# Optimization experiments

Hardware: AMD Instinct MI355X
Metric: run time of the kernel (lower is better)

## Reference

```python
import jax, jax.numpy as jnp
import numpy as np

P_DROP = 0.7   # weights_dropout p
TAU = 0.95     # instance_dropout (gumbel-softmax temperature)


def _linear_init(key, fan_in, fan_out):
    k1, k2 = jax.random.split(key)
    bound = 1.0 / np.sqrt(fan_in)
    W = jax.random.uniform(k1, (fan_in, fan_out), minval=-bound, maxval=bound, dtype=jnp.float32)
    b = jax.random.uniform(k2, (fan_out,), minval=-bound, maxval=bound, dtype=jnp.float32)
    return W, b


def setup_inputs() -> dict:
    key = jax.random.key(0)
    ks = jax.random.split(key, 12)
    N, C, IND = 2048, 64, 512            # Nmol, Nconf, input feature dim
    HD1, HD2, HD3 = 256, 256, 128        # ndim[1:]
    DET1, DET2 = 128, 64                 # det_ndim
    W1, b1 = _linear_init(ks[0], IND, HD1)
    W2, b2 = _linear_init(ks[1], HD1, HD2)
    W3, b3 = _linear_init(ks[2], HD2, HD3)
    D1, db1 = _linear_init(ks[3], HD3, DET1)
    D2, db2 = _linear_init(ks[4], DET1, DET2)
    D3, db3 = _linear_init(ks[5], DET2, 1)
    E, eb = _linear_init(ks[6], HD3, 1)
    x = jax.random.normal(ks[7], (N, C, IND), dtype=jnp.float32)
    m = jnp.ones((N, C, 1), jnp.float32)
    u = jax.random.uniform(ks[8], (N, 1, C), minval=1e-6, maxval=1.0 - 1e-6, dtype=jnp.float32)
    return dict(x=x, m=m, u=u, W1=W1, b1=b1, W2=W2, b2=b2, W3=W3, b3=b3,
                D1=D1, db1=db1, D2=D2, db2=db2, D3=D3, db3=db3, E=E, eb=eb)


def _weights_dropout(w, p):
    # w: (N, 1, C). Zero the lowest p fraction per row, renormalize the rest
    # with a softmax over the kept values (faithful to WeightsDropout.forward).
    N, _, C = w.shape
    k = int(C * p)
    w2 = w[:, 0, :]                                   # (N, C)
    idx = jnp.argsort(w2, axis=1)[:, :k]              # lowest-k indices per row
    keep = jnp.ones_like(w2).at[jnp.arange(N)[:, None], idx].set(0.0)
    masked = jnp.where(keep > 0, w2, -jnp.inf)
    sm = jax.nn.softmax(masked, axis=1)               # softmax over kept values only
    return jnp.where(keep > 0, sm, 0.0)[:, None, :]   # (N, 1, C)


def reference(x, m, u, W1, b1, W2, b2, W3, b3, D1, db1, D2, db2, D3, db3, E, eb):
    h = jax.nn.relu(x @ W1 + b1)
    h = jaxax_relu2 = jax.nn.relu(h @ W2 + b2)
    h = jax.nn.relu(h @ W3 + b3)                      # (N, C, HD3)
    # Detector: (Linear+Sigmoid) x 2, then Linear -> 1
    d = jax.nn.sigmoid(h @ D1 + db1)
    d = jax.nn.sigmoid(d @ D2 + db2)
    d = d @ D3 + db3                                   # (N, C, 1)
    logits = jnp.swapaxes(m * d, 1, 2)                 # (N, 1, C)
    # gumbel_softmax(tau=TAU, dim=2), soft
    g = -jnp.log(-jnp.log(u))
    w = jax.nn.softmax((logits + g) / TAU, axis=2)
    w = _weights_dropout(w, P_DROP)                    # (N, 1, C)
    agg = jnp.einsum('noc,ncd->nod', w, h)             # bmm, (N, 1, HD3)
    out = (agg @ E + eb).reshape(-1, 1)                # (N, 1)
    return (w, out)
```

## Files before the change

### kernel.cpp

```cpp
#include <hip/hip_runtime.h>
#include <math.h>

#define NBAGS 2048
#define CROWS 64
#define IND   512
#define TAUV  0.95f
#define KDROP 44

typedef _Float16 h8  __attribute__((ext_vector_type(8)));
typedef _Float16 h4  __attribute__((ext_vector_type(4)));
typedef float    f16v __attribute__((ext_vector_type(16)));

#define MFMA16(a, b, c) __builtin_amdgcn_mfma_f32_32x32x16_f16(a, b, c, 0, 0, 0)

__device__ __forceinline__ int frag_roff(int lane, int tile, int t, int nkt) {
  return (tile * nkt + t) * 528 + (lane & 31) * 8 + (lane >> 5) * 264;
}

#define W1HI 0
#define W1LO 135168
#define W2HI 270336
#define W2LO 337920
#define W3HI 405504
#define W3LO 439296
#define D1HI 473088
#define D1LO 489984
#define D2HI 506880
#define D2LO 515328
#define WS_ELS 523776

__global__ __launch_bounds__(256) void prep_weights(
    const float* __restrict__ W1, const float* __restrict__ W2,
    const float* __restrict__ W3, const float* __restrict__ D1,
    const float* __restrict__ D2, _Float16* __restrict__ ws)
{
  int e = blockIdx.x * 256 + threadIdx.x;
  const float* src; int local, nlog, nkt, offH, offL;
  if (e < 131072)      { src = W1; local = e;          nlog = 8; nkt = 32; offH = W1HI; offL = W1LO; }
  else if (e < 196608) { src = W2; local = e - 131072; nlog = 8; nkt = 16; offH = W2HI; offL = W2LO; }
  else if (e < 229376) { src = W3; local = e - 196608; nlog = 7; nkt = 16; offH = W3HI; offL = W3LO; }
  else if (e < 245760) { src = D1; local = e - 229376; nlog = 7; nkt = 8;  offH = D1HI; offL = D1LO; }
  else if (e < 253952) { src = D2; local = e - 245760; nlog = 6; nkt = 8;  offH = D2HI; offL = D2LO; }
  else return;
  int k = local >> nlog;
  int n = local & ((1 << nlog) - 1);
  float w = src[local];
  _Float16 hi = (_Float16)w;
  _Float16 lo = (_Float16)(w - (float)hi);
  int addr = ((n >> 5) * nkt + (k >> 4)) * 528 + (n & 31) * 8 + ((k >> 3) & 1) * 264 + (k & 7);
  ws[offH + addr] = hi;
  ws[offL + addr] = lo;
}

template<int NKT_TOT, int NTILES, int KS, int ACT>
__device__ __forceinline__ void gemm_phase(
    const _Float16* __restrict__ bHi, const _Float16* __restrict__ bLo,
    const float* __restrict__ bias,
    const _Float16* aHi, const _Float16* aLo,
    _Float16* oHi, _Float16* oLo, float4* scratch,
    int wave, int lane)
{
  constexpr int TILES = 2 * NTILES;
  constexpr int NKTP  = NKT_TOT / KS;
  constexpr int ONKT  = NTILES * 2;
  const int tile = wave & (TILES - 1);
  const int kh   = wave / TILES;
  const int mt = tile & 1, nt = tile >> 1;
  f16v acc = {};
  if (kh < KS) {
    const int t0 = kh * NKTP;
    h8 bhc, blc, bhn, bln, ahc, alc;
    { int bo = frag_roff(lane, nt, t0, NKT_TOT);
      bhc = *(const h8*)(bHi + bo); blc = *(const h8*)(bLo + bo); }
    if constexpr (NKTP > 1) {
      int bo = frag_roff(lane, nt, t0 + 1, NKT_TOT);
      bhn = *(const h8*)(bHi + bo); bln = *(const h8*)(bLo + bo);
    }
    { int ao = frag_roff(lane, mt, t0, NKT_TOT);
      ahc = *(const h8*)(aHi + ao); alc = *(const h8*)(aLo + ao); }
#pragma unroll
    for (int t = 0; t < NKTP; ++t) {
      h8 bhf, blf, ahn, aln;
      if (t + 2 < NKTP) {
        int bo = frag_roff(lane, nt, t0 + t + 2, NKT_TOT);
        bhf = *(const h8*)(bHi + bo); blf = *(const h8*)(bLo + bo);
      }
      if (t + 1 < NKTP) {
        int ao = frag_roff(lane, mt, t0 + t + 1, NKT_TOT);
        ahn = *(const h8*)(aHi + ao); aln = *(const h8*)(aLo + ao);
      }
      acc = MFMA16(ahc, bhc, acc);
      acc = MFMA16(ahc, blc, acc);
      acc = MFMA16(alc, bhc, acc);
      bhc = bhn; blc = bln; bhn = bhf; bln = blf; ahc = ahn; alc = aln;
    }
  }
  if constexpr (KS > 1) {
    if (kh >= 1 && kh < KS) {
#pragma unroll
      for (int r = 0; r < 4; ++r) {
        float4 v = { acc[4*r], acc[4*r+1], acc[4*r+2], acc[4*r+3] };
        scratch[((tile * (KS - 1) + (kh - 1)) * 4 + r) * 64 + lane] = v;
      }
    }
    __syncthreads();
    if (kh == 0) {
#pragma unroll
      for (int s = 0; s < KS - 1; ++s)
#pragma unroll
        for (int r = 0; r < 4; ++r) {
          float4 v = scratch[((tile * (KS - 1) + s) * 4 + r) * 64 + lane];
          acc[4*r] += v.x; acc[4*r+1] += v.y; acc[4*r+2] += v.z; acc[4*r+3] += v.w;
        }
    }
  }
  if (kh == 0) {
    int n = nt * 32 + (lane & 31);
    float bs = bias[n];
    int t2 = n >> 4, kg = (n >> 3) & 1, j = n & 7;
#pragma unroll
    for (int r = 0; r < 16; ++r) {
      int row = (r & 3) + 8 * (r >> 2) + 4 * (lane >> 5);
      int m = mt * 32 + row;
      float v = acc[r] + bs;
      v = (ACT == 0) ? fmaxf(v, 0.0f) : (1.0f / (1.0f + expf(-v)));
      _Float16 hi = (_Float16)v;
      _Float16 lo = (_Float16)(v - (float)hi);
      int addr = ((m >> 5) * ONKT + t2) * 528 + (m & 31) * 8 + kg * 264 + j;
      oHi[addr] = hi;
      oLo[addr] = lo;
    }
  }
  __syncthreads();
}

__device__ __forceinline__ void phase1(
    const float* __restrict__ xg,
    const _Float16* __restrict__ bHi, const _Float16* __restrict__ bLo,
    const float* __restrict__ bias,
    _Float16* xs,
    _Float16* oHi, _Float16* oLo,
    int tid, int wave, int lane)
{
  const int mt = wave & 1, nt = wave >> 1;
  f16v acc = {};
  float4 xv[2];

  auto loadx = [&](int c) {
#pragma unroll
    for (int it = 0; it < 2; ++it) {
      int flat = it * 1024 + tid;
      int row = flat >> 5, c4 = flat & 31;
      xv[it] = *(const float4*)(xg + row * 512 + c * 128 + c4 * 4);
    }
  };
  auto storex = [&](int c) {
    _Float16* sHi = xs + (c & 1) * 16896;
    _Float16* sLo = sHi + 8448;
#pragma unroll
    for (int it = 0; it < 2; ++it) {
      int flat = it * 1024 + tid;
      int row = flat >> 5, c4 = flat & 31;
      int t = c4 >> 2, kg = (c4 >> 1) & 1, j0 = (c4 & 1) * 4;
      int addr = ((row >> 5) * 8 + t) * 528 + (row & 31) * 8 + kg * 264 + j0;
      float4 v = xv[it];
      h4 hi, lo;
      hi[0] = (_Float16)v.x; lo[0] = (_Float16)(v.x - (float)hi[0]);
      hi[1] = (_Float16)v.y; lo[1] = (_Float16)(v.y - (float)hi[1]);
      hi[2] = (_Float16)v.z; lo[2] = (_Float16)(v.z - (float)hi[2]);
      hi[3] = (_Float16)v.w; lo[3] = (_Float16)(v.w - (float)hi[3]);
      *(h4*)(sHi + addr) = hi;
      *(h4*)(sLo + addr) = lo;
    }
  };

  h8 bhc, blc, bhn, bln;
  { int bo = frag_roff(lane, nt, 0, 32);
    bhc = *(const h8*)(bHi + bo); blc = *(const h8*)(bLo + bo); }
  { int bo = frag_roff(lane, nt, 1, 32);
    bhn = *(const h8*)(bHi + bo); bln = *(const h8*)(bLo + bo); }

  loadx(0);
  storex(0);
  __syncthreads();
  for (int c = 0; c < 4; ++c) {
    if (c < 3) loadx(c + 1);
    const _Float16* sHi = xs + (c & 1) * 16896;
    const _Float16* sLo = sHi + 8448;
    h8 ahc, alc;
    { int ao = frag_roff(lane, mt, 0, 8);
      ahc = *(const h8*)(sHi + ao); alc = *(const h8*)(sLo + ao); }
#pragma unroll
    for (int t = 0; t < 8; ++t) {
      int tg = c * 8 + t;
      h8 bhf, blf, ahn, aln;
      if (tg + 2 < 32) {
        int bo = frag_roff(lane, nt, tg + 2, 32);
        bhf = *(const h8*)(bHi + bo); blf = *(const h8*)(bLo + bo);
      }
      if (t + 1 < 8) {
        int ao = frag_roff(lane, mt, t + 1, 8);
        ahn = *(const h8*)(sHi + ao); aln = *(const h8*)(sLo + ao);
      }
      acc = MFMA16(ahc, bhc, acc);
      acc = MFMA16(ahc, blc, acc);
      acc = MFMA16(alc, bhc, acc);
      bhc = bhn; blc = bln; bhn = bhf; bln = blf; ahc = ahn; alc = aln;
    }
    if (c < 3) storex(c + 1);
    __syncthreads();
  }
  int n = nt * 32 + (lane & 31);
  float bs = bias[n];
  int t2 = n >> 4, kg = (n >> 3) & 1, j = n & 7;
#pragma unroll
  for (int r = 0; r < 16; ++r) {
    int row = (r & 3) + 8 * (r >> 2) + 4 * (lane >> 5);
    int m = mt * 32 + row;
    float v = fmaxf(acc[r] + bs, 0.0f);
    _Float16 hi = (_Float16)v;
    _Float16 lo = (_Float16)(v - (float)hi);
    int addr = ((m >> 5) * 16 + t2) * 528 + (m & 31) * 8 + kg * 264 + j;
    oHi[addr] = hi;
    oLo[addr] = lo;
  }
  __syncthreads();
}

#define BUFB 33792

__global__ __launch_bounds__(1024, 4) void bagnet_mfma(
    const float* __restrict__ gx, const float* __restrict__ gm,
    const float* __restrict__ gu,
    const float* __restrict__ gb1, const float* __restrict__ gb2,
    const float* __restrict__ gb3, const float* __restrict__ gdb1,
    const float* __restrict__ gdb2, const float* __restrict__ gD3,
    const float* __restrict__ gdb3, const float* __restrict__ gE,
    const float* __restrict__ geb, const _Float16* __restrict__ ws,
    float* __restrict__ outw, float* __restrict__ outv)
{
  extern __shared__ _Float16 lds[];
  __shared__ float sZ[64], sEx[64], sW2s[64], sKeep[64], sE2[64], sWf[64], sRed[128];
  const int tid = threadIdx.x, bag = blockIdx.x;
  const int wave = tid >> 6, lane = tid & 63;
  _Float16* bufA = lds;
  _Float16* bufB = lds + BUFB;

  phase1(gx + (size_t)bag * CROWS * IND, ws + W1HI, ws + W1LO, gb1,
         bufB, bufA, bufA + 16896, tid, wave, lane);
  gemm_phase<16, 8, 1, 0>(ws + W2HI, ws + W2LO, gb2, bufA, bufA + 16896,
                          bufB, bufB + 16896, (float4*)bufA, wave, lane);
  gemm_phase<16, 4, 2, 0>(ws + W3HI, ws + W3LO, gb3, bufB, bufB + 16896,
                          bufA, bufA + 8448, (float4*)(bufA + 16896), wave, lane);
  gemm_phase<8, 4, 2, 1>(ws + D1HI, ws + D1LO, gdb1, bufA, bufA + 8448,
                         bufB, bufB + 8448, (float4*)(bufB + 16896), wave, lane);
  gemm_phase<8, 2, 2, 1>(ws + D2HI, ws + D2LO, gdb2, bufB, bufB + 8448,
                         bufA + 16896, bufA + 21120, (float4*)(bufA + 25344), wave, lane);

  const _Float16* d2H = bufA + 16896;
  const _Float16* d2L = bufA + 21120;
  const _Float16* hH  = bufA;
  const _Float16* hL  = bufA + 8448;

  if (tid < CROWS) {
    float a = gdb3[0];
    for (int k = 0; k < 64; ++k) {
      int addr = ((tid >> 5) * 4 + (k >> 4)) * 528 + (tid & 31) * 8 + ((k >> 3) & 1) * 264 + (k & 7);
      a = fmaf((float)d2H[addr] + (float)d2L[addr], gD3[k], a);
    }
    float logit = gm[(size_t)bag * CROWS + tid] * a;
    float uu = gu[(size_t)bag * CROWS + tid];
    float g = -logf(-logf(uu));
    sZ[tid] = (logit + g) * (1.0f / TAUV);
  }
  __syncthreads();
  if (tid < CROWS) {
    float mx = -1e30f;
    for (int j = 0; j < CROWS; ++j) mx = fmaxf(mx, sZ[j]);
    sEx[tid] = expf(sZ[tid] - mx);
  }
  __syncthreads();
  float w2 = 0.0f;
  if (tid < CROWS) {
    float s = 0.0f;
    for (int j = 0; j < CROWS; ++j) s += sEx[j];
    w2 = sEx[tid] / s;
    sW2s[tid] = w2;
  }
  __syncthreads();
  int keep = 0;
  if (tid < CROWS) {
    int cnt = 0;
    for (int j = 0; j < CROWS; ++j) {
      float vj = sW2s[j];
      cnt += (vj < w2) || (vj == w2 && j < tid);
    }
    keep = (cnt >= KDROP) ? 1 : 0;
    sKeep[tid] = (float)keep;
  }
  __syncthreads();
  float e2 = 0.0f;
  if (tid < CROWS) {
    float mk = -1e30f;
    for (int j = 0; j < CROWS; ++j)
      if (sKeep[j] > 0.5f) mk = fmaxf(mk, sW2s[j]);
    e2 = keep ? expf(w2 - mk) : 0.0f;
    sE2[tid] = e2;
  }
  __syncthreads();
  if (tid < CROWS) {
    float s2 = 0.0f;
    for (int j = 0; j < CROWS; ++j) s2 += sE2[j];
    float wf = keep ? (e2 / s2) : 0.0f;
    sWf[tid] = wf;
    outw[(size_t)bag * CROWS + tid] = wf;
  }
  __syncthreads();
  if (tid < 128) {
    float a = 0.0f;
    for (int r = 0; r < CROWS; ++r) {
      int addr = ((r >> 5) * 8 + (tid >> 4)) * 528 + (r & 31) * 8 + ((tid >> 3) & 1) * 264 + (tid & 7);
      a = fmaf(sWf[r], (float)hH[addr] + (float)hL[addr], a);
    }
    sRed[tid] = a * gE[tid];
  }
  __syncthreads();
  if (tid == 0) {
    float s = geb[0];
    for (int j = 0; j < 128; ++j) s += sRed[j];
    outv[bag] = s;
  }
}

extern "C" void kernel_launch(void* const* d_in, const int* in_sizes, int n_in,
                              void* d_out, int out_size, void* d_ws, size_t ws_size,
                              hipStream_t stream) {
  (void)in_sizes; (void)n_in; (void)out_size; (void)ws_size;
  const float* x   = (const float*)d_in[0];
  const float* m   = (const float*)d_in[1];
  const float* u   = (const float*)d_in[2];
  const float* W1  = (const float*)d_in[3];
  const float* b1  = (const float*)d_in[4];
  const float* W2  = (const float*)d_in[5];
  const float* b2  = (const float*)d_in[6];
  const float* W3  = (const float*)d_in[7];
  const float* b3  = (const float*)d_in[8];
  const float* D1  = (const float*)d_in[9];
  const float* db1 = (const float*)d_in[10];
  const float* D2  = (const float*)d_in[11];
  const float* db2 = (const float*)d_in[12];
  const float* D3  = (const float*)d_in[13];
  const float* db3 = (const float*)d_in[14];
  const float* E   = (const float*)d_in[15];
  const float* eb  = (const float*)d_in[16];
  float* outw = (float*)d_out;
  float* outv = outw + (size_t)NBAGS * CROWS;
  _Float16* ws = (_Float16*)d_ws;

  prep_weights<<<992, 256, 0, stream>>>(W1, W2, W3, D1, D2, ws);

  const size_t smem = 2 * (size_t)BUFB * sizeof(_Float16);
  (void)hipFuncSetAttribute((const void*)bagnet_mfma,
                            hipFuncAttributeMaxDynamicSharedMemorySize, (int)smem);
  bagnet_mfma<<<NBAGS, 1024, smem, stream>>>(
      x, m, u, b1, b2, b3, db1, db2, D3, db3, E, eb, ws, outw, outv);
}
```

Measured before the change: 662.0 us.

## Drop split-K reduction and reuse one in-place LDS buffer to raise occupancy

```diff
diff --git a/kernel.cpp b/kernel.cpp
--- a/kernel.cpp
+++ b/kernel.cpp
@@ -52,41 +52,39 @@
   ws[offL + addr] = lo;
 }
 
-template<int NKT_TOT, int NTILES, int KS, int ACT>
+template<int NKT_TOT, int NTILES, int ACT>
 __device__ __forceinline__ void gemm_phase(
     const _Float16* __restrict__ bHi, const _Float16* __restrict__ bLo,
     const float* __restrict__ bias,
     const _Float16* aHi, const _Float16* aLo,
-    _Float16* oHi, _Float16* oLo, float4* scratch,
+    _Float16* oHi, _Float16* oLo,
     int wave, int lane)
 {
   constexpr int TILES = 2 * NTILES;
-  constexpr int NKTP  = NKT_TOT / KS;
   constexpr int ONKT  = NTILES * 2;
   const int tile = wave & (TILES - 1);
   const int kh   = wave / TILES;
   const int mt = tile & 1, nt = tile >> 1;
   f16v acc = {};
-  if (kh < KS) {
-    const int t0 = kh * NKTP;
+  if (kh == 0) {
     h8 bhc, blc, bhn, bln, ahc, alc;
-    { int bo = frag_roff(lane, nt, t0, NKT_TOT);
+    { int bo = frag_roff(lane, nt, 0, NKT_TOT);
       bhc = *(const h8*)(bHi + bo); blc = *(const h8*)(bLo + bo); }
-    if constexpr (NKTP > 1) {
-      int bo = frag_roff(lane, nt, t0 + 1, NKT_TOT);
+    if constexpr (NKT_TOT > 1) {
+      int bo = frag_roff(lane, nt, 1, NKT_TOT);
       bhn = *(const h8*)(bHi + bo); bln = *(const h8*)(bLo + bo);
     }
-    { int ao = frag_roff(lane, mt, t0, NKT_TOT);
+    { int ao = frag_roff(lane, mt, 0, NKT_TOT);
       ahc = *(const h8*)(aHi + ao); alc = *(const h8*)(aLo + ao); }
 #pragma unroll
-    for (int t = 0; t < NKTP; ++t) {
+    for (int t = 0; t < NKT_TOT; ++t) {
       h8 bhf, blf, ahn, aln;
-      if (t + 2 < NKTP) {
-        int bo = frag_roff(lane, nt, t0 + t + 2, NKT_TOT);
+      if (t + 2 < NKT_TOT) {
+        int bo = frag_roff(lane, nt, t + 2, NKT_TOT);
         bhf = *(const h8*)(bHi + bo); blf = *(const h8*)(bLo + bo);
       }
-      if (t + 1 < NKTP) {
-        int ao = frag_roff(lane, mt, t0 + t + 1, NKT_TOT);
+      if (t + 1 < NKT_TOT) {
+        int ao = frag_roff(lane, mt, t + 1, NKT_TOT);
         ahn = *(const h8*)(aHi + ao); aln = *(const h8*)(aLo + ao);
       }
       acc = MFMA16(ahc, bhc, acc);
@@ -95,25 +93,7 @@
       bhc = bhn; blc = bln; bhn = bhf; bln = blf; ahc = ahn; alc = aln;
     }
   }
-  if constexpr (KS > 1) {
-    if (kh >= 1 && kh < KS) {
-#pragma unroll
-      for (int r = 0; r < 4; ++r) {
-        float4 v = { acc[4*r], acc[4*r+1], acc[4*r+2], acc[4*r+3] };
-        scratch[((tile * (KS - 1) + (kh - 1)) * 4 + r) * 64 + lane] = v;
-      }
-    }
-    __syncthreads();
-    if (kh == 0) {
-#pragma unroll
-      for (int s = 0; s < KS - 1; ++s)
-#pragma unroll
-        for (int r = 0; r < 4; ++r) {
-          float4 v = scratch[((tile * (KS - 1) + s) * 4 + r) * 64 + lane];
-          acc[4*r] += v.x; acc[4*r+1] += v.y; acc[4*r+2] += v.z; acc[4*r+3] += v.w;
-        }
-    }
-  }
+  __syncthreads();
   if (kh == 0) {
     int n = nt * 32 + (lane & 31);
     float bs = bias[n];
@@ -227,9 +207,9 @@
   __syncthreads();
 }
 
-#define BUFB 33792
-
-__global__ __launch_bounds__(1024, 4) void bagnet_mfma(
+#define BUFELS 33792
+
+__global__ __launch_bounds__(1024, 8) void bagnet_mfma(
     const float* __restrict__ gx, const float* __restrict__ gm,
     const float* __restrict__ gu,
     const float* __restrict__ gb1, const float* __restrict__ gb2,
@@ -243,24 +223,22 @@
   __shared__ float sZ[64], sEx[64], sW2s[64], sKeep[64], sE2[64], sWf[64], sRed[128];
   const int tid = threadIdx.x, bag = blockIdx.x;
   const int wave = tid >> 6, lane = tid & 63;
-  _Float16* bufA = lds;
-  _Float16* bufB = lds + BUFB;
 
   phase1(gx + (size_t)bag * CROWS * IND, ws + W1HI, ws + W1LO, gb1,
-         bufB, bufA, bufA + 16896, tid, wave, lane);
-  gemm_phase<16, 8, 1, 0>(ws + W2HI, ws + W2LO, gb2, bufA, bufA + 16896,
-                          bufB, bufB + 16896, (float4*)bufA, wave, lane);
-  gemm_phase<16, 4, 2, 0>(ws + W3HI, ws + W3LO, gb3, bufB, bufB + 16896,
-                          bufA, bufA + 8448, (float4*)(bufA + 16896), wave, lane);
-  gemm_phase<8, 4, 2, 1>(ws + D1HI, ws + D1LO, gdb1, bufA, bufA + 8448,
-                         bufB, bufB + 8448, (float4*)(bufB + 16896), wave, lane);
-  gemm_phase<8, 2, 2, 1>(ws + D2HI, ws + D2LO, gdb2, bufB, bufB + 8448,
-                         bufA + 16896, bufA + 21120, (float4*)(bufA + 25344), wave, lane);
-
-  const _Float16* d2H = bufA + 16896;
-  const _Float16* d2L = bufA + 21120;
-  const _Float16* hH  = bufA;
-  const _Float16* hL  = bufA + 8448;
+         lds, lds, lds + 16896, tid, wave, lane);
+  gemm_phase<16, 8, 0>(ws + W2HI, ws + W2LO, gb2, lds, lds + 16896,
+                       lds, lds + 16896, wave, lane);
+  gemm_phase<16, 4, 0>(ws + W3HI, ws + W3LO, gb3, lds, lds + 16896,
+                       lds, lds + 8448, wave, lane);
+  gemm_phase<8, 4, 1>(ws + D1HI, ws + D1LO, gdb1, lds, lds + 8448,
+                      lds + 16896, lds + 25344, wave, lane);
+  gemm_phase<8, 2, 1>(ws + D2HI, ws + D2LO, gdb2, lds + 16896, lds + 25344,
+                      lds + 16896, lds + 21120, wave, lane);
+
+  const _Float16* d2H = lds + 16896;
+  const _Float16* d2L = lds + 21120;
+  const _Float16* hH  = lds;
+  const _Float16* hL  = lds + 8448;
 
   if (tid < CROWS) {
     float a = gdb3[0];
@@ -359,7 +337,7 @@
 
   prep_weights<<<992, 256, 0, stream>>>(W1, W2, W3, D1, D2, ws);
 
-  const size_t smem = 2 * (size_t)BUFB * sizeof(_Float16);
+  const size_t smem = (size_t)BUFELS * sizeof(_Float16);
   (void)hipFuncSetAttribute((const void*)bagnet_mfma,
                             hipFuncAttributeMaxDynamicSharedMemorySize, (int)smem);
   bagnet_mfma<<<NBAGS, 1024, smem, stream>>>(
```

Result: faster. 548.1 us, median of 2 (-17.2%).

## Halve LDS by in-place layer buffers and use wave shuffles for softmax tail

Applied to the files above, without the earlier changes.

```diff
diff --git a/kernel.cpp b/kernel.cpp
--- a/kernel.cpp
+++ b/kernel.cpp
@@ -52,7 +52,7 @@
   ws[offL + addr] = lo;
 }
 
-template<int NKT_TOT, int NTILES, int KS, int ACT>
+template<int NKT_TOT, int NTILES, int KS, int XBAR, int ACT>
 __device__ __forceinline__ void gemm_phase(
     const _Float16* __restrict__ bHi, const _Float16* __restrict__ bLo,
     const float* __restrict__ bias,
@@ -95,6 +95,7 @@
       bhc = bhn; blc = bln; bhn = bhf; bln = blf; ahc = ahn; alc = aln;
     }
   }
+  __syncthreads();
   if constexpr (KS > 1) {
     if (kh >= 1 && kh < KS) {
 #pragma unroll
@@ -113,6 +114,7 @@
           acc[4*r] += v.x; acc[4*r+1] += v.y; acc[4*r+2] += v.z; acc[4*r+3] += v.w;
         }
     }
+    if constexpr (XBAR) __syncthreads();
   }
   if (kh == 0) {
     int n = nt * 32 + (lane & 31);
@@ -123,7 +125,7 @@
       int row = (r & 3) + 8 * (r >> 2) + 4 * (lane >> 5);
       int m = mt * 32 + row;
       float v = acc[r] + bs;
-      v = (ACT == 0) ? fmaxf(v, 0.0f) : (1.0f / (1.0f + expf(-v)));
+      v = (ACT == 0) ? fmaxf(v, 0.0f) : (1.0f / (1.0f + __expf(-v)));
       _Float16 hi = (_Float16)v;
       _Float16 lo = (_Float16)(v - (float)hi);
       int addr = ((m >> 5) * ONKT + t2) * 528 + (m & 31) * 8 + kg * 264 + j;
@@ -227,9 +229,9 @@
   __syncthreads();
 }
 
-#define BUFB 33792
-
-__global__ __launch_bounds__(1024, 4) void bagnet_mfma(
+#define BUFELS 33792
+
+__global__ __launch_bounds__(1024, 8) void bagnet_mfma(
     const float* __restrict__ gx, const float* __restrict__ gm,
     const float* __restrict__ gu,
     const float* __restrict__ gb1, const float* __restrict__ gb2,
@@ -240,80 +242,67 @@
     float* __restrict__ outw, float* __restrict__ outv)
 {
   extern __shared__ _Float16 lds[];
-  __shared__ float sZ[64], sEx[64], sW2s[64], sKeep[64], sE2[64], sWf[64], sRed[128];
+  __shared__ float sWf[64], sPart[2];
   const int tid = threadIdx.x, bag = blockIdx.x;
   const int wave = tid >> 6, lane = tid & 63;
-  _Float16* bufA = lds;
-  _Float16* bufB = lds + BUFB;
 
   phase1(gx + (size_t)bag * CROWS * IND, ws + W1HI, ws + W1LO, gb1,
-         bufB, bufA, bufA + 16896, tid, wave, lane);
-  gemm_phase<16, 8, 1, 0>(ws + W2HI, ws + W2LO, gb2, bufA, bufA + 16896,
-                          bufB, bufB + 16896, (float4*)bufA, wave, lane);
-  gemm_phase<16, 4, 2, 0>(ws + W3HI, ws + W3LO, gb3, bufB, bufB + 16896,
-                          bufA, bufA + 8448, (float4*)(bufA + 16896), wave, lane);
-  gemm_phase<8, 4, 2, 1>(ws + D1HI, ws + D1LO, gdb1, bufA, bufA + 8448,
-                         bufB, bufB + 8448, (float4*)(bufB + 16896), wave, lane);
-  gemm_phase<8, 2, 2, 1>(ws + D2HI, ws + D2LO, gdb2, bufB, bufB + 8448,
-                         bufA + 16896, bufA + 21120, (float4*)(bufA + 25344), wave, lane);
-
-  const _Float16* d2H = bufA + 16896;
-  const _Float16* d2L = bufA + 21120;
-  const _Float16* hH  = bufA;
-  const _Float16* hL  = bufA + 8448;
-
-  if (tid < CROWS) {
+         lds, lds, lds + 16896, tid, wave, lane);
+  gemm_phase<16, 8, 1, 0, 0>(ws + W2HI, ws + W2LO, gb2, lds, lds + 16896,
+                             lds, lds + 16896, nullptr, wave, lane);
+  gemm_phase<16, 4, 2, 0, 0>(ws + W3HI, ws + W3LO, gb3, lds, lds + 16896,
+                             lds, lds + 8448, (float4*)(lds + 16896), wave, lane);
+  gemm_phase<8, 4, 2, 1, 1>(ws + D1HI, ws + D1LO, gdb1, lds, lds + 8448,
+                            lds + 16896, lds + 25344, (float4*)(lds + 16896), wave, lane);
+  gemm_phase<8, 2, 2, 0, 1>(ws + D2HI, ws + D2LO, gdb2, lds + 16896, lds + 25344,
+                            lds + 16896, lds + 21120, (float4*)(lds + 25344), wave, lane);
+
+  const _Float16* d2H = lds + 16896;
+  const _Float16* d2L = lds + 21120;
+  const _Float16* hH  = lds;
+  const _Float16* hL  = lds + 8448;
+
+  if (wave == 0) {
     float a = gdb3[0];
-    for (int k = 0; k < 64; ++k) {
-      int addr = ((tid >> 5) * 4 + (k >> 4)) * 528 + (tid & 31) * 8 + ((k >> 3) & 1) * 264 + (k & 7);
-      a = fmaf((float)d2H[addr] + (float)d2L[addr], gD3[k], a);
-    }
-    float logit = gm[(size_t)bag * CROWS + tid] * a;
-    float uu = gu[(size_t)bag * CROWS + tid];
+#pragma unroll
+    for (int kg8 = 0; kg8 < 8; ++kg8) {
+      int k0 = kg8 * 8;
+      int addr = ((lane >> 5) * 4 + (k0 >> 4)) * 528 + (lane & 31) * 8 + ((k0 >> 3) & 1) * 264;
+      h8 vh = *(const h8*)(d2H + addr);
+      h8 vl = *(const h8*)(d2L + addr);
+#pragma unroll
+      for (int j = 0; j < 8; ++j)
+        a = fmaf((float)vh[j] + (float)vl[j], gD3[k0 + j], a);
+    }
+    float logit = gm[(size_t)bag * CROWS + lane] * a;
+    float uu = gu[(size_t)bag * CROWS + lane];
     float g = -logf(-logf(uu));
-    sZ[tid] = (logit + g) * (1.0f / TAUV);
-  }
-  __syncthreads();
-  if (tid < CROWS) {
-    float mx = -1e30f;
-    for (int j = 0; j < CROWS; ++j) mx = fmaxf(mx, sZ[j]);
-    sEx[tid] = expf(sZ[tid] - mx);
-  }
-  __syncthreads();
-  float w2 = 0.0f;
-  if (tid < CROWS) {
-    float s = 0.0f;
-    for (int j = 0; j < CROWS; ++j) s += sEx[j];
-    w2 = sEx[tid] / s;
-    sW2s[tid] = w2;
-  }
-  __syncthreads();
-  int keep = 0;
-  if (tid < CROWS) {
+    float z = (logit + g) * (1.0f / TAUV);
+    float mx = z;
+#pragma unroll
+    for (int o = 32; o; o >>= 1) mx = fmaxf(mx, __shfl_xor(mx, o));
+    float ex = __expf(z - mx);
+    float s = ex;
+#pragma unroll
+    for (int o = 32; o; o >>= 1) s += __shfl_xor(s, o);
+    float w2 = ex / s;
     int cnt = 0;
-    for (int j = 0; j < CROWS; ++j) {
-      float vj = sW2s[j];
-      cnt += (vj < w2) || (vj == w2 && j < tid);
-    }
-    keep = (cnt >= KDROP) ? 1 : 0;
-    sKeep[tid] = (float)keep;
-  }
-  __syncthreads();
-  float e2 = 0.0f;
-  if (tid < CROWS) {
-    float mk = -1e30f;
-    for (int j = 0; j < CROWS; ++j)
-      if (sKeep[j] > 0.5f) mk = fmaxf(mk, sW2s[j]);
-    e2 = keep ? expf(w2 - mk) : 0.0f;
-    sE2[tid] = e2;
-  }
-  __syncthreads();
-  if (tid < CROWS) {
-    float s2 = 0.0f;
-    for (int j = 0; j < CROWS; ++j) s2 += sE2[j];
+    for (int j = 0; j < 64; ++j) {
+      float vj = __shfl(w2, j);
+      cnt += (vj < w2) || (vj == w2 && j < lane);
+    }
+    int keep = (cnt >= KDROP) ? 1 : 0;
+    float wk = keep ? w2 : -1e30f;
+    float mk = wk;
+#pragma unroll
+    for (int o = 32; o; o >>= 1) mk = fmaxf(mk, __shfl_xor(mk, o));
+    float e2 = keep ? __expf(w2 - mk) : 0.0f;
+    float s2 = e2;
+#pragma unroll
+    for (int o = 32; o; o >>= 1) s2 += __shfl_xor(s2, o);
     float wf = keep ? (e2 / s2) : 0.0f;
-    sWf[tid] = wf;
-    outw[(size_t)bag * CROWS + tid] = wf;
+    sWf[lane] = wf;
+    outw[(size_t)bag * CROWS + lane] = wf;
   }
   __syncthreads();
   if (tid < 128) {
@@ -322,14 +311,13 @@
       int addr = ((r >> 5) * 8 + (tid >> 4)) * 528 + (r & 31) * 8 + ((tid >> 3) & 1) * 264 + (tid & 7);
       a = fmaf(sWf[r], (float)hH[addr] + (float)hL[addr], a);
     }
-    sRed[tid] = a * gE[tid];
-  }
-  __syncthreads();
-  if (tid == 0) {
-    float s = geb[0];
-    for (int j = 0; j < 128; ++j) s += sRed[j];
-    outv[bag] = s;
-  }
+    float p = a * gE[tid];
+#pragma unroll
+    for (int o = 32; o; o >>= 1) p += __shfl_xor(p, o);
+    if (lane == 0) sPart[wave] = p;
+  }
+  __syncthreads();
+  if (tid == 0) outv[bag] = geb[0] + sPart[0] + sPart[1];
 }
 
 extern "C" void kernel_launch(void* const* d_in, const int* in_sizes, int n_in,
@@ -359,7 +347,7 @@
 
   prep_weights<<<992, 256, 0, stream>>>(W1, W2, W3, D1, D2, ws);
 
-  const size_t smem = 2 * (size_t)BUFB * sizeof(_Float16);
+  const size_t smem = (size_t)BUFELS * sizeof(_Float16);
   (void)hipFuncSetAttribute((const void*)bagnet_mfma,
                             hipFuncAttributeMaxDynamicSharedMemorySize, (int)smem);
   bagnet_mfma<<<NBAGS, 1024, smem, stream>>>(
```

After: 814.0 us. 1.23x slower.
